# Performance work log

Hardware: AMD Instinct MI355X
Metric: run time of the kernel (lower is better)

Reference implementation:

```python
import jax, jax.numpy as jnp
import numpy as np

# ---- module config (init kwargs) ----
EMB = 256
HIDDEN = 256
L, H, P = 4, 8, 4
CH = HIDDEN // H
PADDING_MODE = "zeros"   # 'zeros' or 'border'
ALIGN_CORNERS = False
# feature pyramid level shapes (height, width), static
SHAPES = np.array([[128, 128], [64, 64], [32, 32], [16, 16]], dtype=np.int32)
LEVEL_STARTS = np.concatenate([[0], np.cumsum(SHAPES.prod(-1))[:-1]]).astype(np.int32)

B, N = 8, 1024
I = int(SHAPES.prod(-1).sum())  # 21760


def setup_inputs() -> dict:
    key = jax.random.key(0)
    ks = jax.random.split(key, 8)
    scale = 0.02
    return {
        "img": jax.random.normal(ks[0], (B, I, EMB), jnp.float32),
        "img_shapes": jnp.asarray(SHAPES),
        "queries": jax.random.normal(ks[1], (B, N, EMB), jnp.float32),
        "reference_points": jax.random.uniform(ks[2], (B, N, 2), dtype=jnp.float32),
        "W_img": jax.random.normal(ks[3], (EMB, HIDDEN), jnp.float32) * scale,
        "b_img": jnp.zeros((HIDDEN,), jnp.float32),
        "W_q": jax.random.normal(ks[4], (EMB, H * L * P * 3), jnp.float32) * scale,
        "b_q": jnp.zeros((H * L * P * 3,), jnp.float32),
        "W_out": jax.random.normal(ks[5], (HIDDEN, EMB), jnp.float32) * scale,
        "b_out": jnp.zeros((EMB,), jnp.float32),
    }


def _msda(img, points, attn):
    """Multiscale deformable attention core.
    img:    [B, I, H, CH] flattened pyramid features
    points: [B, N, H, L, P, 2] (x, y) in [0, 1]
    attn:   [B, N, H, L, P]
    returns [B, N, H, CH]
    """
    b, _, h_, ch = img.shape
    n = points.shape[1]
    img_t = img.transpose(0, 2, 1, 3)  # [B, H, I, CH]
    levels = []
    for l in range(L):
        hh, ww = int(SHAPES[l, 0]), int(SHAPES[l, 1])
        start = int(LEVEL_STARTS[l])
        p = points[:, :, :, l]  # [B, N, H, P, 2]
        # grid_sample pixel mapping (after the module's 2*p-1 normalization)
        if ALIGN_CORNERS:
            x = p[..., 0] * (ww - 1)
            y = p[..., 1] * (hh - 1)
        else:
            x = p[..., 0] * ww - 0.5
            y = p[..., 1] * hh - 0.5
        x0 = jnp.floor(x); y0 = jnp.floor(y)
        wx = x - x0;       wy = y - y0
        x0i = x0.astype(jnp.int32); y0i = y0.astype(jnp.int32)
        acc = jnp.zeros((b, h_, n * P, ch), img.dtype)
        corners = [
            (x0i,     y0i,     (1 - wx) * (1 - wy)),
            (x0i + 1, y0i,     wx * (1 - wy)),
            (x0i,     y0i + 1, (1 - wx) * wy),
            (x0i + 1, y0i + 1, wx * wy),
        ]
        for xi, yi, cw in corners:
            if PADDING_MODE == "zeros":
                valid = (xi >= 0) & (xi < ww) & (yi >= 0) & (yi < hh)
                cw = cw * valid.astype(cw.dtype)
            xc = jnp.clip(xi, 0, ww - 1)
            yc = jnp.clip(yi, 0, hh - 1)
            idx = start + yc * ww + xc                              # [B, N, H, P]
            idx_t = idx.transpose(0, 2, 1, 3).reshape(b, h_, n * P)  # [B, H, N*P]
            g = jnp.take_along_axis(img_t, idx_t[..., None], axis=2)  # [B, H, N*P, CH]
            cw_t = cw.transpose(0, 2, 1, 3).reshape(b, h_, n * P, 1)
            acc = acc + cw_t * g
        levels.append(acc.reshape(b, h_, n, P, ch))
    samples = jnp.stack(levels, axis=3)            # [B, H, N, L, P, CH]
    attn_t = attn.transpose(0, 2, 1, 3, 4)          # [B, H, N, L, P]
    return jnp.einsum("bhnlpc,bhnlp->bnhc", samples, attn_t)


def reference(img, img_shapes, queries, reference_points, W_img, b_img, W_q, b_q, W_out, b_out):
    b, i_, _ = img.shape
    n = queries.shape[1]
    qp = (queries @ W_q + b_q).reshape(b, n, H, L, P, 3)
    offsets = qp[..., :2]                            # [B, N, H, L, P, 2]
    attn = jax.nn.softmax(qp[..., 2].reshape(b, n, H, L * P), axis=-1).reshape(b, n, H, L, P)
    img_p = (img @ W_img + b_img).reshape(b, i_, H, CH)
    shapes_f = img_shapes.astype(jnp.float32)        # [L, 2] (h, w)
    # faithful to source: offsets / img_shapes[:, None, :]
    sampling_points = reference_points[:, :, None, None, None, :] + offsets / shapes_f[:, None, :]
    out = _msda(img_p, sampling_points, attn)        # [B, N, H, CH]
    return out.reshape(b, n, HIDDEN) @ W_out + b_out
```

## Files before the change

kernel.cpp:

```cpp
#include <hip/hip_runtime.h>
#include <type_traits>
#include <utility>

#define B_    8
#define NQ_   1024
#define I_    21760
#define EMB_  256
#define HID_  256
#define H_    8
#define CH_   32

typedef float  f32x4  __attribute__((ext_vector_type(4)));
typedef __bf16 bf16x8 __attribute__((ext_vector_type(8)));
typedef short  s16x8  __attribute__((ext_vector_type(8)));

template <typename V, typename = void>
struct bf16_mfma_native : std::false_type {};
template <typename V>
struct bf16_mfma_native<V, std::void_t<decltype(__builtin_amdgcn_mfma_f32_16x16x32_bf16(
    std::declval<V>(), std::declval<V>(), std::declval<f32x4>(), 0, 0, 0))>>
    : std::true_type {};

template <typename V>
__device__ __forceinline__ f32x4 mfma_dispatch(V a, V b, f32x4 c) {
  if constexpr (bf16_mfma_native<V>::value) {
    return __builtin_amdgcn_mfma_f32_16x16x32_bf16(a, b, c, 0, 0, 0);
  } else {
    return __builtin_amdgcn_mfma_f32_16x16x32_bf16(
        __builtin_bit_cast(s16x8, a), __builtin_bit_cast(s16x8, b), c, 0, 0, 0);
  }
}

__device__ __forceinline__ f32x4 MFMA(s16x8 a, s16x8 b, f32x4 c) {
  return mfma_dispatch(__builtin_bit_cast(bf16x8, a), __builtin_bit_cast(bf16x8, b), c);
}

__device__ __forceinline__ unsigned short f2bf(float f) {
  unsigned u = __float_as_uint(f);
  u += 0x7fffu + ((u >> 16) & 1u);
  return (unsigned short)(u >> 16);
}

template <bool OUT_BF16>
__global__ __launch_bounds__(512, 2) void gemm64(
    const float* __restrict__ A, const float* __restrict__ W,
    const float* __restrict__ bias, void* __restrict__ Out,
    const int Mtiles) {
  constexpr int N = 256;
  constexpr int LDSTRIDE = 272;
  __shared__ __align__(16) short lds[2][64 * LDSTRIDE];
  const int tid  = threadIdx.x;
  const int lane = tid & 63;
  const int wave = tid >> 6;
  const int quad = lane >> 4;
  const int ln   = lane & 15;

  s16x8 bfrag[2][8];
  f32x4 bias4[2];
#pragma unroll
  for (int st = 0; st < 2; ++st) {
    const int ng = st * 128 + wave * 16 + ln;
    bias4[st] = *(const f32x4*)&bias[st * 128 + wave * 16 + quad * 4];
#pragma unroll
    for (int ks = 0; ks < 8; ++ks) {
      s16x8 f;
#pragma unroll
      for (int j = 0; j < 8; ++j)
        f[j] = (short)f2bf(W[(ks * 32 + quad * 8 + j) * N + ng]);
      bfrag[st][ks] = f;
    }
  }

  const int srow0 = wave * 8;

  float4 pf[8];
  int t = blockIdx.x;
  {
    const float* Ab = A + (size_t)t * 64 * 256;
#pragma unroll
    for (int j = 0; j < 8; ++j) pf[j] = ((const float4*)Ab)[j * 512 + tid];
#pragma unroll
    for (int j = 0; j < 8; ++j) {
      const int row = j * 8 + wave;
      uint2 u;
      u.x = (unsigned)f2bf(pf[j].x) | ((unsigned)f2bf(pf[j].y) << 16);
      u.y = (unsigned)f2bf(pf[j].z) | ((unsigned)f2bf(pf[j].w) << 16);
      *(uint2*)&lds[0][row * LDSTRIDE + lane * 4] = u;
    }
  }
  __syncthreads();
  (void)srow0;

  int p = 0;
  while (t < Mtiles) {
    const int tn = t + gridDim.x;
    const bool more = (tn < Mtiles);
    if (more) {
      const float* Ab = A + (size_t)tn * 64 * 256;
#pragma unroll
      for (int j = 0; j < 8; ++j) pf[j] = ((const float4*)Ab)[j * 512 + tid];
    }

    f32x4 acc[2][4];
#pragma unroll
    for (int st = 0; st < 2; ++st)
#pragma unroll
      for (int rt = 0; rt < 4; ++rt) acc[st][rt] = bias4[st];

#pragma unroll
    for (int ks = 0; ks < 8; ++ks) {
      s16x8 a[4];
#pragma unroll
      for (int rt = 0; rt < 4; ++rt)
        a[rt] = *(const s16x8*)&lds[p][(rt * 16 + ln) * LDSTRIDE + ks * 32 + quad * 8];
#pragma unroll
      for (int st = 0; st < 2; ++st)
#pragma unroll
        for (int rt = 0; rt < 4; ++rt)
          acc[st][rt] = MFMA(bfrag[st][ks], a[rt], acc[st][rt]);
    }

    const size_t rowBase = (size_t)t * 64;
#pragma unroll
    for (int st = 0; st < 2; ++st) {
      const int col = st * 128 + wave * 16 + quad * 4;
#pragma unroll
      for (int rt = 0; rt < 4; ++rt) {
        const size_t row = rowBase + rt * 16 + ln;
        if constexpr (OUT_BF16) {
          uint2 u;
          u.x = (unsigned)f2bf(acc[st][rt][0]) | ((unsigned)f2bf(acc[st][rt][1]) << 16);
          u.y = (unsigned)f2bf(acc[st][rt][2]) | ((unsigned)f2bf(acc[st][rt][3]) << 16);
          *(uint2*)&((unsigned short*)Out)[row * N + col] = u;
        } else {
          *(f32x4*)&((float*)Out)[row * N + col] = acc[st][rt];
        }
      }
    }

    if (more) {
#pragma unroll
      for (int j = 0; j < 8; ++j) {
        const int row = j * 8 + wave;
        uint2 u;
        u.x = (unsigned)f2bf(pf[j].x) | ((unsigned)f2bf(pf[j].y) << 16);
        u.y = (unsigned)f2bf(pf[j].z) | ((unsigned)f2bf(pf[j].w) << 16);
        *(uint2*)&lds[p ^ 1][row * LDSTRIDE + lane * 4] = u;
      }
      __syncthreads();
    }
    p ^= 1;
    t = tn;
  }
}

__global__ __launch_bounds__(512, 2) void qproj_softmax_kernel(
    const float* __restrict__ A, const float* __restrict__ W,
    const float* __restrict__ bias, const float* __restrict__ refp,
    float* __restrict__ attn, float* __restrict__ pts) {
  constexpr int N = 384;
  __shared__ __align__(16) char smem[32 * 392 * 4];
  short* slds = (short*)smem;
  float* sout = (float*)smem;
  const int tid  = threadIdx.x;
  const int lane = tid & 63;
  const int wave = tid >> 6;
  const int quad = lane >> 4;
  const int ln   = lane & 15;

  s16x8 bfrag[3][8];
  float bv[3];
#pragma unroll
  for (int st = 0; st < 3; ++st) {
    const int ng = st * 128 + wave * 16 + ln;
    bv[st] = bias[ng];
#pragma unroll
    for (int ks = 0; ks < 8; ++ks) {
      s16x8 f;
#pragma unroll
      for (int j = 0; j < 8; ++j)
        f[j] = (short)f2bf(W[(ks * 32 + quad * 8 + j) * N + ng]);
      bfrag[st][ks] = f;
    }
  }

  const size_t rowBase = (size_t)blockIdx.x * 32;
  {
    const float* Ab = A + rowBase * 256;
#pragma unroll
    for (int j = 0; j < 4; ++j) {
      float4 v = ((const float4*)Ab)[j * 512 + tid];
      const int row = j * 8 + wave;
      uint2 u;
      u.x = (unsigned)f2bf(v.x) | ((unsigned)f2bf(v.y) << 16);
      u.y = (unsigned)f2bf(v.z) | ((unsigned)f2bf(v.w) << 16);
      *(uint2*)&slds[row * 264 + lane * 4] = u;
    }
  }
  __syncthreads();

  f32x4 acc[3][2];
#pragma unroll
  for (int st = 0; st < 3; ++st) {
    acc[st][0] = f32x4{bv[st], bv[st], bv[st], bv[st]};
    acc[st][1] = acc[st][0];
  }
#pragma unroll
  for (int ks = 0; ks < 8; ++ks) {
    s16x8 a0 = *(const s16x8*)&slds[ln * 264 + ks * 32 + quad * 8];
    s16x8 a1 = *(const s16x8*)&slds[(ln + 16) * 264 + ks * 32 + quad * 8];
#pragma unroll
    for (int st = 0; st < 3; ++st) {
      acc[st][0] = MFMA(a0, bfrag[st][ks], acc[st][0]);
      acc[st][1] = MFMA(a1, bfrag[st][ks], acc[st][1]);
    }
  }
  __syncthreads();

#pragma unroll
  for (int st = 0; st < 3; ++st) {
    const int ng = st * 128 + wave * 16 + ln;
#pragma unroll
    for (int rt = 0; rt < 2; ++rt)
#pragma unroll
      for (int r = 0; r < 4; ++r)
        sout[(rt * 16 + quad * 4 + r) * 392 + ng] = acc[st][rt][r];
  }
  __syncthreads();

  if (tid < 256) {
    const int ql = tid >> 3, h = tid & 7;
    const float* basep = sout + ql * 392 + h * 48;
    float s[16];
    float mx = -1e30f;
#pragma unroll
    for (int lp = 0; lp < 16; ++lp) {
      s[lp] = basep[lp * 3 + 2];
      mx = fmaxf(mx, s[lp]);
    }
    float sum = 0.f;
#pragma unroll
    for (int lp = 0; lp < 16; ++lp) {
      s[lp] = __expf(s[lp] - mx);
      sum += s[lp];
    }
    const float inv = 1.0f / sum;
    const size_t q   = rowBase + ql;
    const size_t gq8 = q * 8 + h;
    float* ao = attn + gq8 * 16;
#pragma unroll
    for (int lp = 0; lp < 16; ++lp) ao[lp] = s[lp] * inv;

    const float rx = refp[q * 2], ry = refp[q * 2 + 1];
    float* po = pts + gq8 * 32;
    const float invsh[4] = {1.f / 128.f, 1.f / 64.f, 1.f / 32.f, 1.f / 16.f};
#pragma unroll
    for (int l = 0; l < 4; ++l) {
#pragma unroll
      for (int p = 0; p < 4; ++p) {
        const int lp = l * 4 + p;
        po[lp * 2 + 0] = rx + basep[lp * 3 + 0] * invsh[l];
        po[lp * 2 + 1] = ry + basep[lp * 3 + 1] * invsh[l];
      }
    }
  }
}

__global__ __launch_bounds__(256) void msda_sample_kernel(
    const unsigned int* __restrict__ imgp,
    const float* __restrict__ attn, const float* __restrict__ pts,
    float* __restrict__ out) {
  __shared__ __align__(16) float sw[1024][4];
  __shared__ __align__(16) int   sib[1024][4];
  const int bid = blockIdx.x;
  const int tid = threadIdx.x;

#pragma unroll
  for (int it = 0; it < 4; ++it) {
    const int i  = it * 256 + tid;
    const int q  = i >> 7;
    const int h  = (i >> 4) & 7;
    const int lp = i & 15;
    const int l  = lp >> 2;
    const int gq = bid * 8 + q;
    const int b  = gq >> 10;
    const int ww = 128 >> l;
    const int start = (l > 0 ? 16384 : 0) + (l > 1 ? 4096 : 0) + (l > 2 ? 1024 : 0);
    const float2 p = *(const float2*)&pts[((size_t)gq * 8 + h) * 32 + lp * 2];
    const float a  = attn[((size_t)gq * 8 + h) * 16 + lp];
    const float x = p.x * (float)ww - 0.5f;
    const float y = p.y * (float)ww - 0.5f;
    const float x0f = floorf(x), y0f = floorf(y);
    const float wx = x - x0f, wy = y - y0f;
    const int x0 = (int)x0f, y0 = (int)y0f;
    const float cw[4] = {(1.f - wx) * (1.f - wy), wx * (1.f - wy),
                         (1.f - wx) * wy,          wx * wy};
#pragma unroll
    for (int c = 0; c < 4; ++c) {
      const int xi = x0 + (c & 1), yi = y0 + (c >> 1);
      const bool valid = (xi >= 0) & (xi < ww) & (yi >= 0) & (yi < ww);
      const int xc = min(max(xi, 0), ww - 1);
      const int yc = min(max(yi, 0), ww - 1);
      const int idx = start + yc * ww + xc;
      sw[i][c]  = valid ? a * cw[c] : 0.f;
      sib[i][c] = ((b * I_ + idx) << 7) + (h << 4);
    }
  }
  __syncthreads();

  const int q  = tid >> 5;
  const int h  = (tid >> 2) & 7;
  const int c8 = tid & 3;
  float2 acc[4];
#pragma unroll
  for (int k = 0; k < 4; ++k) acc[k] = float2{0.f, 0.f};

#define BFLO(v) __uint_as_float((v) << 16)
#define BFHI(v) __uint_as_float((v) & 0xffff0000u)
#pragma unroll
  for (int lp = 0; lp < 16; ++lp) {
    const int sidx = q * 128 + h * 16 + lp;
    const float4 w4 = *(const float4*)sw[sidx];
    const int4   i4 = *(const int4*)sib[sidx];
    const uint4 u0 = *(const uint4*)&imgp[i4.x + c8 * 4];
    const uint4 u1 = *(const uint4*)&imgp[i4.y + c8 * 4];
    const uint4 u2 = *(const uint4*)&imgp[i4.z + c8 * 4];
    const uint4 u3 = *(const uint4*)&imgp[i4.w + c8 * 4];
#define ACCUM(U, WGT)                                        \
    acc[0].x += (WGT) * BFLO(U.x); acc[0].y += (WGT) * BFHI(U.x); \
    acc[1].x += (WGT) * BFLO(U.y); acc[1].y += (WGT) * BFHI(U.y); \
    acc[2].x += (WGT) * BFLO(U.z); acc[2].y += (WGT) * BFHI(U.z); \
    acc[3].x += (WGT) * BFLO(U.w); acc[3].y += (WGT) * BFHI(U.w);
    ACCUM(u0, w4.x)
    ACCUM(u1, w4.y)
    ACCUM(u2, w4.z)
    ACCUM(u3, w4.w)
#undef ACCUM
  }
#undef BFLO
#undef BFHI

  const int gq = bid * 8 + q;
  float* dst = &out[(size_t)gq * 256 + h * 32 + c8 * 8];
  float4 r0{acc[0].x, acc[0].y, acc[1].x, acc[1].y};
  float4 r1{acc[2].x, acc[2].y, acc[3].x, acc[3].y};
  *(float4*)dst = r0;
  *(float4*)(dst + 4) = r1;
}

#define OFF_IMGP 0ULL
#define OFF_ATTN 89128960ULL
#define OFF_PTS  93323264ULL
#define OFF_MSDA 101711872ULL
#define WS_NEEDED 110100480ULL

extern "C" void kernel_launch(void* const* d_in, const int* in_sizes, int n_in,
                              void* d_out, int out_size, void* d_ws, size_t ws_size,
                              hipStream_t stream) {
  const float* img     = (const float*)d_in[0];
  const float* queries = (const float*)d_in[2];
  const float* refp    = (const float*)d_in[3];
  const float* W_img   = (const float*)d_in[4];
  const float* b_img   = (const float*)d_in[5];
  const float* W_q     = (const float*)d_in[6];
  const float* b_q     = (const float*)d_in[7];
  const float* W_out   = (const float*)d_in[8];
  const float* b_out   = (const float*)d_in[9];

  if (ws_size < WS_NEEDED) return;

  char* ws = (char*)d_ws;
  unsigned short* imgp = (unsigned short*)(ws + OFF_IMGP);
  float* attn = (float*)(ws + OFF_ATTN);
  float* pts  = (float*)(ws + OFF_PTS);
  float* msda = (float*)(ws + OFF_MSDA);

  hipLaunchKernelGGL((gemm64<true>), dim3(256), dim3(512), 0, stream,
                     img, W_img, b_img, (void*)imgp, I_ * B_ / 64);
  hipLaunchKernelGGL(qproj_softmax_kernel, dim3(B_ * NQ_ / 32), dim3(512), 0, stream,
                     queries, W_q, b_q, refp, attn, pts);
  hipLaunchKernelGGL(msda_sample_kernel, dim3(B_ * NQ_ / 8), dim3(256), 0, stream,
                     (const unsigned int*)imgp, attn, pts, msda);
  hipLaunchKernelGGL((gemm64<false>), dim3(128), dim3(512), 0, stream,
                     msda, W_out, b_out, d_out, 128);
}
```

Baseline: 340.6 us.

## Stream GEMM A tiles into LDS as fp32 via global_load_lds with XOR swizzle

Replaces the register-staged prefetch (global load, convert to bf16, write LDS) with direct global-to-LDS async copies of fp32 A tiles using an XOR swizzle to avoid bank conflicts. The bf16 conversion moves to the point where MFMA operands are read from LDS, using the packed hardware conversion intrinsic. This is meant to free registers and VALU work from the prefetch path and overlap the copy better. In exchange it doubles LDS per block (128KB for two fp32 buffers), which may cut occupancy, and makes each tile pay conversion for both of the two output halves.

```diff
diff --git a/kernel.cpp b/kernel.cpp
--- a/kernel.cpp
+++ b/kernel.cpp
@@ -1,4 +1,5 @@
 #include <hip/hip_runtime.h>
+#include <hip/hip_bf16.h>
 #include <type_traits>
 #include <utility>
 
@@ -41,14 +42,28 @@
   return (unsigned short)(u >> 16);
 }
 
+__device__ __forceinline__ s16x8 pack8(f32x4 a, f32x4 b) {
+  union { s16x8 v; __hip_bfloat162 h[4]; } r;
+  r.h[0] = __float22bfloat162_rn(float2{a[0], a[1]});
+  r.h[1] = __float22bfloat162_rn(float2{a[2], a[3]});
+  r.h[2] = __float22bfloat162_rn(float2{b[0], b[1]});
+  r.h[3] = __float22bfloat162_rn(float2{b[2], b[3]});
+  return r.v;
+}
+
+typedef __attribute__((address_space(1))) const void gas_t;
+typedef __attribute__((address_space(3))) void las_t;
+__device__ __forceinline__ void glds16(const void* g, void* l) {
+  __builtin_amdgcn_global_load_lds((gas_t*)g, (las_t*)l, 16, 0, 0);
+}
+
 template <bool OUT_BF16>
-__global__ __launch_bounds__(512, 2) void gemm64(
+__global__ __launch_bounds__(512, 2) void gemm_glds(
     const float* __restrict__ A, const float* __restrict__ W,
     const float* __restrict__ bias, void* __restrict__ Out,
     const int Mtiles) {
   constexpr int N = 256;
-  constexpr int LDSTRIDE = 272;
-  __shared__ __align__(16) short lds[2][64 * LDSTRIDE];
+  __shared__ __align__(16) float buf[2][64 * 256];
   const int tid  = threadIdx.x;
   const int lane = tid & 63;
   const int wave = tid >> 6;
@@ -71,34 +86,30 @@
     }
   }
 
-  const int srow0 = wave * 8;
-
-  float4 pf[8];
+  const int lx16 = (lane ^ wave) << 4;
+
   int t = blockIdx.x;
   {
-    const float* Ab = A + (size_t)t * 64 * 256;
-#pragma unroll
-    for (int j = 0; j < 8; ++j) pf[j] = ((const float4*)Ab)[j * 512 + tid];
+    const char* Ab = (const char*)(A + (size_t)t * 64 * 256);
 #pragma unroll
     for (int j = 0; j < 8; ++j) {
       const int row = j * 8 + wave;
-      uint2 u;
-      u.x = (unsigned)f2bf(pf[j].x) | ((unsigned)f2bf(pf[j].y) << 16);
-      u.y = (unsigned)f2bf(pf[j].z) | ((unsigned)f2bf(pf[j].w) << 16);
-      *(uint2*)&lds[0][row * LDSTRIDE + lane * 4] = u;
-    }
-  }
-  __syncthreads();
-  (void)srow0;
+      glds16(Ab + (size_t)row * 1024 + lx16, &buf[0][row * 256]);
+    }
+  }
+  __syncthreads();
 
   int p = 0;
   while (t < Mtiles) {
     const int tn = t + gridDim.x;
     const bool more = (tn < Mtiles);
     if (more) {
-      const float* Ab = A + (size_t)tn * 64 * 256;
-#pragma unroll
-      for (int j = 0; j < 8; ++j) pf[j] = ((const float4*)Ab)[j * 512 + tid];
+      const char* Ab = (const char*)(A + (size_t)tn * 64 * 256);
+#pragma unroll
+      for (int j = 0; j < 8; ++j) {
+        const int row = j * 8 + wave;
+        glds16(Ab + (size_t)row * 1024 + lx16, &buf[p ^ 1][row * 256]);
+      }
     }
 
     f32x4 acc[2][4];
@@ -107,12 +118,19 @@
 #pragma unroll
       for (int rt = 0; rt < 4; ++rt) acc[st][rt] = bias4[st];
 
+    const float* bp = buf[p];
+    const int key = ln & 7;
 #pragma unroll
     for (int ks = 0; ks < 8; ++ks) {
+      const int cb = ks * 8 + quad * 2;
       s16x8 a[4];
 #pragma unroll
-      for (int rt = 0; rt < 4; ++rt)
-        a[rt] = *(const s16x8*)&lds[p][(rt * 16 + ln) * LDSTRIDE + ks * 32 + quad * 8];
+      for (int rt = 0; rt < 4; ++rt) {
+        const float* rp = bp + (rt * 16 + ln) * 256;
+        f32x4 x0 = *(const f32x4*)&rp[((cb)     ^ key) * 4];
+        f32x4 x1 = *(const f32x4*)&rp[((cb + 1) ^ key) * 4];
+        a[rt] = pack8(x0, x1);
+      }
 #pragma unroll
       for (int st = 0; st < 2; ++st)
 #pragma unroll
@@ -138,17 +156,7 @@
       }
     }
 
-    if (more) {
-#pragma unroll
-      for (int j = 0; j < 8; ++j) {
-        const int row = j * 8 + wave;
-        uint2 u;
-        u.x = (unsigned)f2bf(pf[j].x) | ((unsigned)f2bf(pf[j].y) << 16);
-        u.y = (unsigned)f2bf(pf[j].z) | ((unsigned)f2bf(pf[j].w) << 16);
-        *(uint2*)&lds[p ^ 1][row * LDSTRIDE + lane * 4] = u;
-      }
-      __syncthreads();
-    }
+    if (more) __syncthreads();
     p ^= 1;
     t = tn;
   }
@@ -375,12 +383,12 @@
   float* pts  = (float*)(ws + OFF_PTS);
   float* msda = (float*)(ws + OFF_MSDA);
 
-  hipLaunchKernelGGL((gemm64<true>), dim3(256), dim3(512), 0, stream,
+  hipLaunchKernelGGL((gemm_glds<true>), dim3(256), dim3(512), 0, stream,
                      img, W_img, b_img, (void*)imgp, I_ * B_ / 64);
   hipLaunchKernelGGL(qproj_softmax_kernel, dim3(B_ * NQ_ / 32), dim3(512), 0, stream,
                      queries, W_q, b_q, refp, attn, pts);
   hipLaunchKernelGGL(msda_sample_kernel, dim3(B_ * NQ_ / 8), dim3(256), 0, stream,
                      (const unsigned int*)imgp, attn, pts, msda);
-  hipLaunchKernelGGL((gemm64<false>), dim3(128), dim3(512), 0, stream,
+  hipLaunchKernelGGL((gemm_glds<false>), dim3(128), dim3(512), 0, stream,
                      msda, W_out, b_out, d_out, 128);
 }
```

Result: no change. 341.3 us (+0.2%).
